# Kernel tuning notes

Hardware: AMD Instinct MI355X
Metric: run time of the kernel (lower is better)

Reference implementation:

```python
import jax, jax.numpy as jnp
import numpy as np

N, K = 50000, 20
NUM_RELS, INP_DIM, SEM_DIM = 200, 64, 32
PAD = NUM_RELS  # padding_idx row of rel_emb (zeros)


def setup_inputs() -> dict:
    key = jax.random.key(0)
    k1, k2, k3, k4, k5, k6 = jax.random.split(key, 6)
    out_nei_rels = jax.random.randint(k1, (N, K), 0, NUM_RELS + 1)
    in_nei_rels = jax.random.randint(k2, (N, K), 0, NUM_RELS + 1)
    target_rels = jax.random.randint(k3, (N,), 0, NUM_RELS)
    feat = jax.random.normal(k4, (N, INP_DIM - SEM_DIM), dtype=jnp.float32)
    rel_emb = jax.random.normal(k5, (NUM_RELS + 1, INP_DIM), dtype=jnp.float32)
    rel_emb = rel_emb.at[PAD].set(0.0)  # padding_idx row is zero
    w_rel2ent_w = jax.random.normal(k6, (SEM_DIM, 2 * INP_DIM), dtype=jnp.float32) / np.sqrt(2 * INP_DIM)
    w_rel2ent_b = jnp.zeros((SEM_DIM,), dtype=jnp.float32)
    return {
        "out_nei_rels": out_nei_rels,
        "in_nei_rels": in_nei_rels,
        "target_rels": target_rels,
        "feat": feat,
        "rel_emb": rel_emb,
        "w_rel2ent_w": w_rel2ent_w,
        "w_rel2ent_b": w_rel2ent_b,
    }


def reference(out_nei_rels, in_nei_rels, target_rels, feat, rel_emb, w_rel2ent_w, w_rel2ent_b):
    # Gather per-node neighbor-relation embeddings: [N, K, D]
    out_e = rel_emb[out_nei_rels]
    in_e = rel_emb[in_nei_rels]
    tgt = rel_emb[target_rels]  # [N, D]
    # Attention scores against the target relation, softmax over K neighbors.
    # (dropout is identity in eval mode / rate 0)
    out_att = jax.nn.softmax(jnp.einsum("nkd,nd->nk", out_e, tgt), axis=1)
    in_att = jax.nn.softmax(jnp.einsum("nkd,nd->nk", in_e, tgt), axis=1)
    # Attention-weighted aggregation of neighbor-relation embeddings: [N, D]
    out_sem = jnp.einsum("nk,nkd->nd", out_att, out_e)
    in_sem = jnp.einsum("nk,nkd->nd", in_att, in_e)
    # init_nei_rels == 'both': linear + sigmoid on concatenated sem feats
    sem = jnp.concatenate([out_sem, in_sem], axis=1)  # [N, 2D]
    ent_sem_feats = jax.nn.sigmoid(sem @ w_rel2ent_w.T + w_rel2ent_b)  # [N, sem_dim]
    return jnp.concatenate([feat, ent_sem_feats], axis=1)  # g.ndata['init']
```

## Files before the change

kernel.cpp:

```cpp
#include <hip/hip_runtime.h>
#include <hip/hip_fp16.h>

#define N_REL 201
#define N_TGT 200
#define SEM 32
#define KNEI 20
#define PSTRIDE 40

#define S_BYTES 80400
#define S_U4 (S_BYTES / 16)
#define P_HALFS (2 * N_REL * PSTRIDE)
#define P_U4 (P_HALFS * 2 / 16)

__global__ __launch_bounds__(256) void build_tables_kernel(
    const float* __restrict__ rel_emb,
    const float* __restrict__ w,
    const float* __restrict__ bias,
    __half* __restrict__ S,
    __half* __restrict__ P)
{
  __shared__ float embL[N_REL * 65];
  __shared__ float wL[SEM * 129];
  const int t = threadIdx.x;
  for (int e = t; e < N_REL * 64; e += 256) {
    int r = e >> 6, d = e & 63;
    embL[r * 65 + d] = rel_emb[e];
  }
  for (int e = t; e < SEM * 128; e += 256) {
    int r = e >> 7, c = e & 127;
    wL[r * 129 + c] = w[e];
  }
  __syncthreads();

  const int i = blockIdx.x;
  for (int jj = t; jj < N_TGT; jj += 256) {
    float acc = 0.f;
#pragma unroll
    for (int d = 0; d < 64; ++d)
      acc = fmaf(embL[i * 65 + d], embL[jj * 65 + d], acc);
    S[i * N_TGT + jj] = __float2half(acc);
  }
  if (t < 64) {
    int hh = t >> 5, jj = t & 31;
    float acc = 0.5f * bias[jj];
#pragma unroll
    for (int d = 0; d < 64; ++d)
      acc = fmaf(embL[i * 65 + d], wL[jj * 129 + hh * 64 + d], acc);
    P[(hh * N_REL + i) * PSTRIDE + jj] = __float2half(acc);
  }
}

__global__ __launch_bounds__(1024, 4) void fuse_kernel(
    const int* __restrict__ out_nei, const int* __restrict__ in_nei,
    const int* __restrict__ target, const float* __restrict__ feat,
    const __half* __restrict__ Sg, const __half* __restrict__ Pg,
    float* __restrict__ out, int n_nodes)
{
  __shared__ __align__(16) __half S_l[S_U4 * 8];
  __shared__ __align__(16) __half P_l[P_HALFS];
  const int t = threadIdx.x;
  {
    const uint4* s4 = (const uint4*)Sg;
    uint4* sl = (uint4*)S_l;
    for (int e = t; e < S_U4; e += 1024) sl[e] = s4[e];
    const uint4* p4 = (const uint4*)Pg;
    uint4* pl = (uint4*)P_l;
    for (int e = t; e < P_U4; e += 1024) pl[e] = p4[e];
  }
  __syncthreads();

  const int gid = blockIdx.x * 1024 + t;
  const int n = gid >> 2;
  if (n >= n_nodes) return;
  const int sub = t & 3;
  const int dir = sub >> 1;
  const int h = sub & 1;

  const int tgt = target[n];
  const int* __restrict__ nei = dir ? in_nei : out_nei;

  int idxA[KNEI];
#pragma unroll
  for (int r = 0; r < 5; ++r) {
    const uint4 v = ((const uint4*)(nei + (size_t)n * KNEI))[r];
    idxA[4 * r + 0] = (int)v.x;
    idxA[4 * r + 1] = (int)v.y;
    idxA[4 * r + 2] = (int)v.z;
    idxA[4 * r + 3] = (int)v.w;
  }
  float ev[KNEI];
#pragma unroll
  for (int k = 0; k < KNEI; ++k)
    ev[k] = __half2float(S_l[idxA[k] * N_TGT + tgt]);
  float mx = ev[0];
#pragma unroll
  for (int k = 1; k < KNEI; ++k) mx = fmaxf(mx, ev[k]);
  float s = 0.f;
#pragma unroll
  for (int k = 0; k < KNEI; ++k) {
    ev[k] = __expf(ev[k] - mx);
    s += ev[k];
  }
  const float inv = __fdividef(1.f, s);

  __half2 acc[8];
#pragma unroll
  for (int m = 0; m < 8; ++m) acc[m] = __float2half2_rn(0.f);
#pragma unroll
  for (int k = 0; k < KNEI; ++k) {
    const __half2 a2 = __float2half2_rn(ev[k] * inv);
    const int rb = (dir * N_REL + idxA[k]) * PSTRIDE + h * 16;
    const uint4 q0 = *(const uint4*)&P_l[rb];
    const uint4 q1 = *(const uint4*)&P_l[rb + 8];
    acc[0] = __hfma2(a2, *(const __half2*)&q0.x, acc[0]);
    acc[1] = __hfma2(a2, *(const __half2*)&q0.y, acc[1]);
    acc[2] = __hfma2(a2, *(const __half2*)&q0.z, acc[2]);
    acc[3] = __hfma2(a2, *(const __half2*)&q0.w, acc[3]);
    acc[4] = __hfma2(a2, *(const __half2*)&q1.x, acc[4]);
    acc[5] = __hfma2(a2, *(const __half2*)&q1.y, acc[5]);
    acc[6] = __hfma2(a2, *(const __half2*)&q1.z, acc[6]);
    acc[7] = __hfma2(a2, *(const __half2*)&q1.w, acc[7]);
  }
  float tv[16];
#pragma unroll
  for (int m = 0; m < 8; ++m) {
    const unsigned int u = *(const unsigned int*)&acc[m];
    const unsigned int v = __shfl_xor(u, 2, 64);
    const __half2 tot = __hadd2(acc[m], *(const __half2*)&v);
    tv[2 * m]     = __low2float(tot);
    tv[2 * m + 1] = __high2float(tot);
  }

  float* orow = out + (size_t)n * 64;
  if (dir) {
    float4 sg[4];
#pragma unroll
    for (int r = 0; r < 4; ++r) {
      sg[r].x = __fdividef(1.f, 1.f + __expf(-tv[4 * r + 0]));
      sg[r].y = __fdividef(1.f, 1.f + __expf(-tv[4 * r + 1]));
      sg[r].z = __fdividef(1.f, 1.f + __expf(-tv[4 * r + 2]));
      sg[r].w = __fdividef(1.f, 1.f + __expf(-tv[4 * r + 3]));
    }
#pragma unroll
    for (int r = 0; r < 4; ++r)
      ((float4*)(orow + SEM + h * 16))[r] = sg[r];
  } else {
    const float4* frow = (const float4*)(feat + (size_t)n * SEM + h * 16);
#pragma unroll
    for (int r = 0; r < 4; ++r)
      ((float4*)(orow + h * 16))[r] = frow[r];
  }
}

extern "C" void kernel_launch(void* const* d_in, const int* in_sizes, int n_in,
                              void* d_out, int out_size, void* d_ws, size_t ws_size,
                              hipStream_t stream) {
  const int* out_nei   = (const int*)d_in[0];
  const int* in_nei    = (const int*)d_in[1];
  const int* target    = (const int*)d_in[2];
  const float* feat    = (const float*)d_in[3];
  const float* rel_emb = (const float*)d_in[4];
  const float* w       = (const float*)d_in[5];
  const float* bias    = (const float*)d_in[6];
  float* out = (float*)d_out;
  const int n_nodes = in_sizes[2];

  __half* S = (__half*)d_ws;
  __half* P = (__half*)((char*)d_ws + S_BYTES);

  build_tables_kernel<<<N_REL, 256, 0, stream>>>(rel_emb, w, bias, S, P);
  const int threads_total = n_nodes * 4;
  const int nb = (threads_total + 1023) / 1024;
  fuse_kernel<<<nb, 1024, 0, stream>>>(out_nei, in_nei, target, feat, S, P,
                                       out, n_nodes);
}
```

Baseline: 23.00 us.

## Drop shared score table, gather transposed scores from global, split nodes across eight lanes

After: 22.56 us. Within noise of the previous version (-1.9%).

```diff
diff --git a/kernel.cpp b/kernel.cpp
--- a/kernel.cpp
+++ b/kernel.cpp
@@ -7,8 +7,7 @@
 #define KNEI 20
 #define PSTRIDE 40
 
-#define S_BYTES 80400
-#define S_U4 (S_BYTES / 16)
+#define ST_BYTES 80400
 #define P_HALFS (2 * N_REL * PSTRIDE)
 #define P_U4 (P_HALFS * 2 / 16)
 
@@ -16,7 +15,7 @@
     const float* __restrict__ rel_emb,
     const float* __restrict__ w,
     const float* __restrict__ bias,
-    __half* __restrict__ S,
+    __half* __restrict__ St,
     __half* __restrict__ P)
 {
   __shared__ float embL[N_REL * 65];
@@ -38,7 +37,7 @@
 #pragma unroll
     for (int d = 0; d < 64; ++d)
       acc = fmaf(embL[i * 65 + d], embL[jj * 65 + d], acc);
-    S[i * N_TGT + jj] = __float2half(acc);
+    St[jj * N_REL + i] = __float2half(acc);
   }
   if (t < 64) {
     int hh = t >> 5, jj = t & 31;
@@ -50,105 +49,121 @@
   }
 }
 
-__global__ __launch_bounds__(1024, 4) void fuse_kernel(
+__global__ __launch_bounds__(256, 5) void fuse_kernel(
     const int* __restrict__ out_nei, const int* __restrict__ in_nei,
     const int* __restrict__ target, const float* __restrict__ feat,
-    const __half* __restrict__ Sg, const __half* __restrict__ Pg,
+    const __half* __restrict__ St, const __half* __restrict__ Pg,
     float* __restrict__ out, int n_nodes)
 {
-  __shared__ __align__(16) __half S_l[S_U4 * 8];
   __shared__ __align__(16) __half P_l[P_HALFS];
   const int t = threadIdx.x;
+  const int gid = blockIdx.x * 256 + t;
+  const int n = gid >> 3;
+  const int sub = t & 7;
+  const int dir = sub >> 2;
+  const int q = sub & 3;
+  const bool active = (n < n_nodes);
+
+  int tgt = 0;
+  int idxA[5];
+  float4 f0, f1;
+  if (active) {
+    tgt = target[n];
+    const int* __restrict__ nei = dir ? in_nei : out_nei;
+#pragma unroll
+    for (int i = 0; i < 5; ++i) idxA[i] = nei[(size_t)n * KNEI + q * 5 + i];
+    if (dir == 0) {
+      const float4* frow = (const float4*)(feat + (size_t)n * SEM + q * 8);
+      f0 = frow[0];
+      f1 = frow[1];
+    }
+  }
+
   {
-    const uint4* s4 = (const uint4*)Sg;
-    uint4* sl = (uint4*)S_l;
-    for (int e = t; e < S_U4; e += 1024) sl[e] = s4[e];
     const uint4* p4 = (const uint4*)Pg;
     uint4* pl = (uint4*)P_l;
-    for (int e = t; e < P_U4; e += 1024) pl[e] = p4[e];
+    for (int e = t; e < P_U4; e += 256) pl[e] = p4[e];
   }
   __syncthreads();
+  if (!active) return;
 
-  const int gid = blockIdx.x * 1024 + t;
-  const int n = gid >> 2;
-  if (n >= n_nodes) return;
-  const int sub = t & 3;
-  const int dir = sub >> 1;
-  const int h = sub & 1;
+  float ev[5];
+  const __half* __restrict__ srow = St + (size_t)tgt * N_REL;
+#pragma unroll
+  for (int i = 0; i < 5; ++i) ev[i] = __half2float(srow[idxA[i]]);
 
-  const int tgt = target[n];
-  const int* __restrict__ nei = dir ? in_nei : out_nei;
-
-  int idxA[KNEI];
-#pragma unroll
-  for (int r = 0; r < 5; ++r) {
-    const uint4 v = ((const uint4*)(nei + (size_t)n * KNEI))[r];
-    idxA[4 * r + 0] = (int)v.x;
-    idxA[4 * r + 1] = (int)v.y;
-    idxA[4 * r + 2] = (int)v.z;
-    idxA[4 * r + 3] = (int)v.w;
-  }
-  float ev[KNEI];
-#pragma unroll
-  for (int k = 0; k < KNEI; ++k)
-    ev[k] = __half2float(S_l[idxA[k] * N_TGT + tgt]);
   float mx = ev[0];
 #pragma unroll
-  for (int k = 1; k < KNEI; ++k) mx = fmaxf(mx, ev[k]);
+  for (int i = 1; i < 5; ++i) mx = fmaxf(mx, ev[i]);
+  mx = fmaxf(mx, __shfl_xor(mx, 1, 64));
+  mx = fmaxf(mx, __shfl_xor(mx, 2, 64));
   float s = 0.f;
 #pragma unroll
-  for (int k = 0; k < KNEI; ++k) {
-    ev[k] = __expf(ev[k] - mx);
-    s += ev[k];
+  for (int i = 0; i < 5; ++i) {
+    ev[i] = __expf(ev[i] - mx);
+    s += ev[i];
   }
+  s += __shfl_xor(s, 1, 64);
+  s += __shfl_xor(s, 2, 64);
   const float inv = __fdividef(1.f, s);
 
-  __half2 acc[8];
+  unsigned int pk[20];
 #pragma unroll
-  for (int m = 0; m < 8; ++m) acc[m] = __float2half2_rn(0.f);
+  for (int i = 0; i < 5; ++i) {
+    const __half hw = __float2half(ev[i] * inv);
+    pk[i] = ((unsigned int)idxA[i] << 16) | (unsigned int)__half_as_ushort(hw);
+  }
 #pragma unroll
-  for (int k = 0; k < KNEI; ++k) {
-    const __half2 a2 = __float2half2_rn(ev[k] * inv);
-    const int rb = (dir * N_REL + idxA[k]) * PSTRIDE + h * 16;
-    const uint4 q0 = *(const uint4*)&P_l[rb];
-    const uint4 q1 = *(const uint4*)&P_l[rb + 8];
-    acc[0] = __hfma2(a2, *(const __half2*)&q0.x, acc[0]);
-    acc[1] = __hfma2(a2, *(const __half2*)&q0.y, acc[1]);
-    acc[2] = __hfma2(a2, *(const __half2*)&q0.z, acc[2]);
-    acc[3] = __hfma2(a2, *(const __half2*)&q0.w, acc[3]);
-    acc[4] = __hfma2(a2, *(const __half2*)&q1.x, acc[4]);
-    acc[5] = __hfma2(a2, *(const __half2*)&q1.y, acc[5]);
-    acc[6] = __hfma2(a2, *(const __half2*)&q1.z, acc[6]);
-    acc[7] = __hfma2(a2, *(const __half2*)&q1.w, acc[7]);
-  }
-  float tv[16];
+  for (int i = 0; i < 5; ++i) pk[5 + i] = __shfl_xor(pk[i], 1, 64);
 #pragma unroll
-  for (int m = 0; m < 8; ++m) {
-    const unsigned int u = *(const unsigned int*)&acc[m];
-    const unsigned int v = __shfl_xor(u, 2, 64);
-    const __half2 tot = __hadd2(acc[m], *(const __half2*)&v);
-    tv[2 * m]     = __low2float(tot);
-    tv[2 * m + 1] = __high2float(tot);
+  for (int i = 0; i < 10; ++i) pk[10 + i] = __shfl_xor(pk[i], 2, 64);
+
+  __half2 acc[4];
+#pragma unroll
+  for (int m = 0; m < 4; ++m) acc[m] = __float2half2_rn(0.f);
+  const int dbase = dir * (N_REL * PSTRIDE) + q * 8;
+#pragma unroll
+  for (int i = 0; i < 20; ++i) {
+    const int idx = (int)(pk[i] >> 16);
+    const unsigned int lo = pk[i] & 0xFFFFu;
+    const unsigned int dd = lo | (lo << 16);
+    const __half2 a2 = *(const __half2*)&dd;
+    const uint4 qv = *(const uint4*)&P_l[dbase + idx * PSTRIDE];
+    acc[0] = __hfma2(a2, *(const __half2*)&qv.x, acc[0]);
+    acc[1] = __hfma2(a2, *(const __half2*)&qv.y, acc[1]);
+    acc[2] = __hfma2(a2, *(const __half2*)&qv.z, acc[2]);
+    acc[3] = __hfma2(a2, *(const __half2*)&qv.w, acc[3]);
   }
 
-  float* orow = out + (size_t)n * 64;
-  if (dir) {
-    float4 sg[4];
 #pragma unroll
-    for (int r = 0; r < 4; ++r) {
-      sg[r].x = __fdividef(1.f, 1.f + __expf(-tv[4 * r + 0]));
-      sg[r].y = __fdividef(1.f, 1.f + __expf(-tv[4 * r + 1]));
-      sg[r].z = __fdividef(1.f, 1.f + __expf(-tv[4 * r + 2]));
-      sg[r].w = __fdividef(1.f, 1.f + __expf(-tv[4 * r + 3]));
+  for (int m = 0; m < 4; ++m) {
+    const unsigned int u = *(const unsigned int*)&acc[m];
+    const unsigned int v = __shfl_xor(u, 4, 64);
+    acc[m] = __hadd2(acc[m], *(const __half2*)&v);
+  }
+
+  float* orow = out + (size_t)n * 64 + sub * 8;
+  if (dir == 0) {
+    ((float4*)orow)[0] = f0;
+    ((float4*)orow)[1] = f1;
+  } else {
+    float tv[8];
+#pragma unroll
+    for (int m = 0; m < 4; ++m) {
+      tv[2 * m]     = __low2float(acc[m]);
+      tv[2 * m + 1] = __high2float(acc[m]);
     }
-#pragma unroll
-    for (int r = 0; r < 4; ++r)
-      ((float4*)(orow + SEM + h * 16))[r] = sg[r];
-  } else {
-    const float4* frow = (const float4*)(feat + (size_t)n * SEM + h * 16);
-#pragma unroll
-    for (int r = 0; r < 4; ++r)
-      ((float4*)(orow + h * 16))[r] = frow[r];
+    float4 s0, s1;
+    s0.x = __fdividef(1.f, 1.f + __expf(-tv[0]));
+    s0.y = __fdividef(1.f, 1.f + __expf(-tv[1]));
+    s0.z = __fdividef(1.f, 1.f + __expf(-tv[2]));
+    s0.w = __fdividef(1.f, 1.f + __expf(-tv[3]));
+    s1.x = __fdividef(1.f, 1.f + __expf(-tv[4]));
+    s1.y = __fdividef(1.f, 1.f + __expf(-tv[5]));
+    s1.z = __fdividef(1.f, 1.f + __expf(-tv[6]));
+    s1.w = __fdividef(1.f, 1.f + __expf(-tv[7]));
+    ((float4*)orow)[0] = s0;
+    ((float4*)orow)[1] = s1;
   }
 }
 
@@ -165,12 +180,12 @@
   float* out = (float*)d_out;
   const int n_nodes = in_sizes[2];
 
-  __half* S = (__half*)d_ws;
-  __half* P = (__half*)((char*)d_ws + S_BYTES);
+  __half* St = (__half*)d_ws;
+  __half* P  = (__half*)((char*)d_ws + ST_BYTES);
 
-  build_tables_kernel<<<N_REL, 256, 0, stream>>>(rel_emb, w, bias, S, P);
-  const int threads_total = n_nodes * 4;
-  const int nb = (threads_total + 1023) / 1024;
-  fuse_kernel<<<nb, 1024, 0, stream>>>(out_nei, in_nei, target, feat, S, P,
-                                       out, n_nodes);
+  build_tables_kernel<<<N_REL, 256, 0, stream>>>(rel_emb, w, bias, St, P);
+  const int total_threads = n_nodes * 8;
+  const int nb = (total_threads + 255) / 256;
+  fuse_kernel<<<nb, 256, 0, stream>>>(out_nei, in_nei, target, feat, St, P,
+                                      out, n_nodes);
 }
```
